# Performance work log

Hardware: AMD Instinct MI355X
Metric: run time of the kernel (lower is better)

The kernel has to match this reference:

```python
import jax, jax.numpy as jnp
import numpy as np

ROI = 268
K = 32
SLOPE = 0.33
EPS = 1e-5

def leaky(h):
    return jnp.where(h >= 0, h, SLOPE * h)

def bn(h, g, b):
    # BatchNorm in training mode: biased batch statistics over the node/batch axis
    mu = h.mean(0)
    var = ((h - mu) ** 2).mean(0)
    return (h - mu) * jax.lax.rsqrt(var + EPS) * g + b


def setup_inputs():
    B, F, C, deg = 64, ROI, 32, 32
    N = B * ROI
    key = jax.random.key(0)
    ks = jax.random.split(key, 32)
    x = jax.random.normal(ks[0], (N, F), jnp.float32)
    # static within-graph edges: every node has exactly `deg` incoming edges
    tgt = jnp.repeat(jnp.arange(N, dtype=jnp.int32), deg)
    src = (tgt // ROI) * ROI + jax.random.randint(ks[1], (N * deg,), 0, ROI, dtype=jnp.int32)
    edge_index = jnp.stack([src, tgt])
    batch = jnp.repeat(jnp.arange(B, dtype=jnp.int32), ROI)
    def lin(k, i, o):
        return 0.05 * jax.random.normal(k, (i, o), jnp.float32)
    def vec(k, o):
        return 0.05 * jax.random.normal(k, (o,), jnp.float32)
    p = dict(
        x=x, edge_index=edge_index, batch=batch,
        W1a=lin(ks[2], 2 * F, C), b1a=vec(ks[3], C), W1b=lin(ks[4], C, C), b1b=vec(ks[5], C),
        g1=1.0 + vec(ks[6], C), be1=vec(ks[7], C),
        W2a=lin(ks[8], 2 * F, C), b2a=vec(ks[9], C), W2b=lin(ks[10], C, C), b2b=vec(ks[11], C),
        g2=1.0 + vec(ks[12], C), be2=vec(ks[13], C),
        W3=lin(ks[14], 2 * F, 1), b3=vec(ks[15], 1), g3=1.0 + vec(ks[16], 1), be3=vec(ks[17], 1),
        Wl1=lin(ks[18], ROI + 2 * C, 256), bl1=vec(ks[19], 256), g4=1.0 + vec(ks[20], 256), be4=vec(ks[21], 256),
        Wl2=lin(ks[22], 256, 128), bl2=vec(ks[23], 128), g5=1.0 + vec(ks[24], 128), be5=vec(ks[25], 128),
        Wl3=lin(ks[26], 128, 1), bl3=vec(ks[27], 1),
    )
    return p


def reference(x, edge_index, batch,
              W1a, b1a, W1b, b1b, g1, be1,
              W2a, b2a, W2b, b2b, g2, be2,
              W3, b3, g3, be3,
              Wl1, bl1, g4, be4, Wl2, bl2, g5, be5, Wl3, bl3):
    N, F = x.shape
    B = N // ROI
    src, tgt = edge_index[0], edge_index[1]
    xi = x[tgt]                       # [E, F] central node feature
    xd = x[src] - xi                  # [E, F] x_j - x_i
    # --- gcn1: EdgeConv(mlp1) + BN + LeakyReLU (dropout = identity in eval) ---
    m1 = leaky(xi @ W1a[:F] + xd @ W1a[F:] + b1a) @ W1b + b1b   # [E, C]
    a1 = jax.ops.segment_max(m1, tgt, num_segments=N)
    a1 = jnp.where(jnp.isfinite(a1), a1, 0.0)
    x1 = leaky(bn(a1, g1, be1))
    # --- gcn3: EdgeConv(mlp3) + BN + LeakyReLU ---
    m3 = xi @ W3[:F] + xd @ W3[F:] + b3                          # [E, 1]
    a3 = jax.ops.segment_max(m3, tgt, num_segments=N)
    a3 = jnp.where(jnp.isfinite(a3), a3, 0.0)
    x3 = leaky(bn(a3, g3, be3))
    # --- gcn2: DynamicEdgeConv(mlp2, k=32) + BN + LeakyReLU ---
    xg = x.reshape(B, ROI, F)
    sq = jnp.sum(xg * xg, -1)
    d2 = sq[:, :, None] + sq[:, None, :] - 2.0 * jnp.einsum('bif,bjf->bij', xg, xg)
    _, idx = jax.lax.top_k(-d2, K)                               # [B, ROI, K], includes self
    xj = jax.vmap(lambda f, i: f[i])(xg, idx)                    # [B, ROI, K, F]
    part_i = jnp.einsum('bif,fc->bic', xg, W2a[:F])
    part_d = jnp.einsum('bikf,fc->bikc', xj - xg[:, :, None, :], W2a[F:])
    h2 = leaky(part_i[:, :, None, :] + part_d + b2a)
    m2 = h2 @ W2b + b2b                                          # [B, ROI, K, C]
    x2 = leaky(bn(m2.max(axis=2).reshape(N, -1), g2, be2))
    # --- readout ---
    counts = jax.ops.segment_sum(jnp.ones((N, 1), x.dtype), batch, num_segments=B)
    p1 = jax.ops.segment_sum(x1, batch, num_segments=B) / counts
    p2 = jax.ops.segment_sum(x2, batch, num_segments=B) / counts
    z = jnp.concatenate([p1, p2, x3.reshape(B, ROI)], -1)        # [B, 268+64]
    z = leaky(bn(z @ Wl1 + bl1, g4, be4))
    z = leaky(bn(z @ Wl2 + bl2, g5, be5))
    return z @ Wl3 + bl3                                          # [B, 1]
```

## Files before the change

### kernel.cpp

```cpp
#include <hip/hip_runtime.h>
#include <hip/hip_bf16.h>

#define ROI   268
#define FDIM  268
#define NB    64
#define NN    (NB*ROI)
#define CC    32
#define DEG   32
#define KSEL  32
#define SLOPE 0.33f
#define EPSBN 1e-5f

typedef __attribute__((ext_vector_type(8)))  short bf16x8;
typedef __attribute__((ext_vector_type(4)))  float f32x4;
typedef __attribute__((ext_vector_type(16))) float f32x16;

__device__ __forceinline__ float lrelu(float h) { return h >= 0.f ? h : SLOPE * h; }

__device__ __forceinline__ unsigned short f2bf(float f) {
    union { __hip_bfloat16 h; unsigned short s; } u;
    u.h = __float2bfloat16(f);
    return u.s;
}
__device__ __forceinline__ float bf2f(unsigned short h) {
    return __uint_as_float(((unsigned int)h) << 16);
}

#define PREP_PACK_BLOCKS  2448
#define PREP_PACKW_BLOCKS 18
#define PREP_SCAL_BLOCKS  1072

__global__ __launch_bounds__(256) void k_prep(
    const float* __restrict__ x,
    const float* __restrict__ W1a, const float* __restrict__ W2a,
    const float* __restrict__ W3,  const float* __restrict__ b3,
    unsigned short* __restrict__ Xh, unsigned short* __restrict__ Xl,
    unsigned short* __restrict__ Wfh, unsigned short* __restrict__ Wfl,
    float* __restrict__ u3, float* __restrict__ v3, float* __restrict__ sqv)
{
    const int bid = blockIdx.x;
    const int tid = threadIdx.x;
    if (bid < PREP_PACK_BLOCKS) {
        const int gid = bid * 256 + tid;
        const int l   = gid & 63;
        const int f3  = gid >> 6;
        const int ks  = f3 % 9;
        const int bc  = f3 / 9;
        const int ct  = bc % 17;
        const int b   = bc / 17;
        const int node = ct * 16 + (l & 15);
        const int k0   = ks * 32 + (l >> 4) * 8;
        float f[8];
        #pragma unroll
        for (int j = 0; j < 8; ++j) f[j] = 0.f;
        if (node < ROI) {
            const float* row = &x[((size_t)b * ROI + node) * FDIM];
            if (k0 + 3 < FDIM) { float4 v = *(const float4*)&row[k0];     f[0]=v.x; f[1]=v.y; f[2]=v.z; f[3]=v.w; }
            if (k0 + 7 < FDIM) { float4 v = *(const float4*)&row[k0 + 4]; f[4]=v.x; f[5]=v.y; f[6]=v.z; f[7]=v.w; }
        }
        unsigned short hh[8], ll[8];
        #pragma unroll
        for (int j = 0; j < 8; ++j) {
            hh[j] = f2bf(f[j]);
            ll[j] = f2bf(f[j] - bf2f(hh[j]));
        }
        uint4 hp, lp;
        hp.x = (unsigned)hh[0] | ((unsigned)hh[1] << 16); hp.y = (unsigned)hh[2] | ((unsigned)hh[3] << 16);
        hp.z = (unsigned)hh[4] | ((unsigned)hh[5] << 16); hp.w = (unsigned)hh[6] | ((unsigned)hh[7] << 16);
        lp.x = (unsigned)ll[0] | ((unsigned)ll[1] << 16); lp.y = (unsigned)ll[2] | ((unsigned)ll[3] << 16);
        lp.z = (unsigned)ll[4] | ((unsigned)ll[5] << 16); lp.w = (unsigned)ll[6] | ((unsigned)ll[7] << 16);
        const size_t base = (size_t)f3 * 512 + l * 8;
        *(uint4*)&Xh[base] = hp;
        *(uint4*)&Xl[base] = lp;
    } else if (bid < PREP_PACK_BLOCKS + PREP_PACKW_BLOCKS) {
        const int gid = (bid - PREP_PACK_BLOCKS) * 256 + tid;
        const int l  = gid & 63;
        const int f3 = gid >> 6;
        const int ks = f3 % 9;
        const int mc = f3 / 9;
        const int ct = mc & 1;
        const int m  = mc >> 1;
        const int k0 = ks * 32 + (l >> 4) * 8;
        const int c  = ct * 16 + (l & 15);
        const float* W = (m < 2) ? W1a : W2a;
        const bool isU = (m & 1) == 0;
        unsigned short hh[8], ll[8];
        #pragma unroll
        for (int j = 0; j < 8; ++j) {
            const int kk = k0 + j;
            float val = 0.f;
            if (kk < FDIM) {
                float wb = W[(size_t)(FDIM + kk) * CC + c];
                val = isU ? (W[(size_t)kk * CC + c] - wb) : wb;
            }
            hh[j] = f2bf(val);
            ll[j] = f2bf(val - bf2f(hh[j]));
        }
        uint4 hp, lp;
        hp.x = (unsigned)hh[0] | ((unsigned)hh[1] << 16); hp.y = (unsigned)hh[2] | ((unsigned)hh[3] << 16);
        hp.z = (unsigned)hh[4] | ((unsigned)hh[5] << 16); hp.w = (unsigned)hh[6] | ((unsigned)hh[7] << 16);
        lp.x = (unsigned)ll[0] | ((unsigned)ll[1] << 16); lp.y = (unsigned)ll[2] | ((unsigned)ll[3] << 16);
        lp.z = (unsigned)ll[4] | ((unsigned)ll[5] << 16); lp.w = (unsigned)ll[6] | ((unsigned)ll[7] << 16);
        const size_t base = (size_t)f3 * 512 + l * 8;
        *(uint4*)&Wfh[base] = hp;
        *(uint4*)&Wfl[base] = lp;
    } else {
        const int s = bid - (PREP_PACK_BLOCKS + PREP_PACKW_BLOCKS);
        const int l = tid & 63;
        #pragma unroll
        for (int i = 0; i < 4; ++i) {
            const int n = s * 16 + i * 4 + (tid >> 6);
            const float* row = &x[(size_t)n * FDIM];
            float su = 0.f, sv = 0.f, sq = 0.f;
            #pragma unroll
            for (int t = 0; t < 4; ++t) {
                const int f = l + 64 * t;
                float xv = row[f];
                float wv = W3[FDIM + f];
                float wu = W3[f] - wv;
                su += xv * wu; sv += xv * wv; sq += xv * xv;
            }
            if (l < 12) {
                const int f = 256 + l;
                float xv = row[f];
                float wv = W3[FDIM + f];
                float wu = W3[f] - wv;
                su += xv * wu; sv += xv * wv; sq += xv * xv;
            }
            #pragma unroll
            for (int mm = 32; mm > 0; mm >>= 1) {
                su += __shfl_xor(su, mm);
                sv += __shfl_xor(sv, mm);
                sq += __shfl_xor(sq, mm);
            }
            if (l == 0) {
                u3[n] = su + b3[0];
                v3[n] = sv;
                sqv[n] = sq;
            }
        }
    }
}

__global__ __launch_bounds__(256) void k_proj_mfma(
    const unsigned short* __restrict__ Xh, const unsigned short* __restrict__ Xl,
    const unsigned short* __restrict__ Wfh, const unsigned short* __restrict__ Wfl,
    const float* __restrict__ b1a, const float* __restrict__ b2a,
    float* __restrict__ u1, float* __restrict__ v1,
    float* __restrict__ u2, float* __restrict__ v2)
{
    const int tid = threadIdx.x;
    const int l   = tid & 63;
    const int m   = tid >> 6;
    const int tile = blockIdx.x;
    const int b    = tile / 17;
    const int ctn  = tile % 17;

    bf16x8 Ah[9], Al[9];
    {
        const size_t abase = (size_t)tile * 9 * 512 + l * 8;
        #pragma unroll
        for (int ks = 0; ks < 9; ++ks) {
            Ah[ks] = *(const bf16x8*)&Xh[abase + ks * 512];
            Al[ks] = *(const bf16x8*)&Xl[abase + ks * 512];
        }
    }
    float* outp = (m == 0) ? u1 : (m == 1) ? v1 : (m == 2) ? u2 : v2;

    #pragma unroll
    for (int ct = 0; ct < 2; ++ct) {
        const size_t wbase = ((size_t)((m * 2 + ct) * 9)) * 512 + l * 8;
        f32x4 acc = {0.f, 0.f, 0.f, 0.f};
        #pragma unroll
        for (int ks = 0; ks < 9; ++ks) {
            bf16x8 bh = *(const bf16x8*)&Wfh[wbase + ks * 512];
            bf16x8 bl = *(const bf16x8*)&Wfl[wbase + ks * 512];
            acc = __builtin_amdgcn_mfma_f32_16x16x32_bf16(Ah[ks], bh, acc, 0, 0, 0);
            acc = __builtin_amdgcn_mfma_f32_16x16x32_bf16(Ah[ks], bl, acc, 0, 0, 0);
            acc = __builtin_amdgcn_mfma_f32_16x16x32_bf16(Al[ks], bh, acc, 0, 0, 0);
        }
        const int ch = ct * 16 + (l & 15);
        float bias = 0.f;
        if (m == 0) bias = b1a[ch];
        else if (m == 2) bias = b2a[ch];
        const int r0 = (l >> 4) * 4;
        #pragma unroll
        for (int i = 0; i < 4; ++i) {
            const int node = ctn * 16 + r0 + i;
            if (node < ROI)
                outp[((size_t)b * ROI + node) * 32 + ch] = acc[i] + bias;
        }
    }
}

__global__ __launch_bounds__(256) void k_dist(
    const unsigned short* __restrict__ Xh, const unsigned short* __restrict__ Xl,
    const float* __restrict__ sqv, float* __restrict__ d2)
{
    __shared__ float sqj[288];
    __shared__ float sqr[32];
    const int tid = threadIdx.x;
    const int b   = blockIdx.y;
    const int r0g = blockIdx.x * 32;
    const size_t bN = (size_t)b * ROI;

    for (int t = tid; t < 288; t += 256)
        sqj[t] = (t < ROI) ? sqv[bN + t] : __builtin_inff();
    if (tid < 32) sqr[tid] = (r0g + tid < ROI) ? sqv[bN + r0g + tid] : 0.f;

    const int l  = tid & 63;
    const int w  = tid >> 6;
    const int ra = w & 1;
    const int rtile = min(blockIdx.x * 2 + ra, 16);

    bf16x8 Ah[9], Al[9];
    {
        const size_t abase = ((size_t)(b * 17 + rtile) * 9) * 512 + l * 8;
        #pragma unroll
        for (int ks = 0; ks < 9; ++ks) {
            Ah[ks] = *(const bf16x8*)&Xh[abase + ks * 512];
            Al[ks] = *(const bf16x8*)&Xl[abase + ks * 512];
        }
    }
    __syncthreads();

    float* drow = &d2[(size_t)b * 288 * 288];
    for (int ct = (w >> 1); ct < 17; ct += 2) {
        const size_t bbase = ((size_t)(b * 17 + ct) * 9) * 512 + l * 8;
        f32x4 acc = {0.f, 0.f, 0.f, 0.f};
        #pragma unroll
        for (int ks = 0; ks < 9; ++ks) {
            bf16x8 bh = *(const bf16x8*)&Xh[bbase + ks * 512];
            bf16x8 bl = *(const bf16x8*)&Xl[bbase + ks * 512];
            acc = __builtin_amdgcn_mfma_f32_16x16x32_bf16(Ah[ks], bh, acc, 0, 0, 0);
            acc = __builtin_amdgcn_mfma_f32_16x16x32_bf16(Ah[ks], bl, acc, 0, 0, 0);
            acc = __builtin_amdgcn_mfma_f32_16x16x32_bf16(Al[ks], bh, acc, 0, 0, 0);
        }
        const int col = ct * 16 + (l & 15);
        const float sj = sqj[col];
        const int rr = ra * 16 + (l >> 4) * 4;
        #pragma unroll
        for (int i = 0; i < 4; ++i)
            drow[(size_t)(r0g + rr + i) * 288 + col] = sqr[rr + i] + sj - 2.f * acc[i];
    }
    for (int t = tid; t < 32 * 16; t += 256) {
        const int r = t >> 4, cc = 272 + (t & 15);
        drow[(size_t)(r0g + r) * 288 + cc] = __builtin_inff();
    }
}

__global__ __launch_bounds__(256) void k_sel(
    const float* __restrict__ d2, int* __restrict__ knn)
{
    const int grp = blockIdx.x * 8 + (threadIdx.x >> 5);
    const int sl  = threadIdx.x & 31;
    const int b   = grp / ROI;
    const int row = grp - b * ROI;
    const float* src = &d2[((size_t)b * 288 + row) * 288];

    unsigned k[9];
    #pragma unroll
    for (int q = 0; q < 9; ++q) {
        const int idx = q * 32 + sl;
        unsigned bits = __float_as_uint(src[idx]);
        unsigned msk  = (unsigned)(((int)bits) >> 31) | 0x80000000u;
        k[q] = ((bits ^ msk) & ~0x1FFu) | (unsigned)idx;
    }
    #pragma unroll
    for (int i = 1; i < 9; ++i) {
        #pragma unroll
        for (int j = i; j > 0; --j) {
            unsigned lo = k[j-1] < k[j] ? k[j-1] : k[j];
            unsigned hi = k[j-1] < k[j] ? k[j]   : k[j-1];
            k[j-1] = lo; k[j] = hi;
        }
    }
    unsigned keep = 0;
    #pragma unroll
    for (int it = 0; it < KSEL; ++it) {
        unsigned m = k[0];
        #pragma unroll
        for (int mm = 16; mm > 0; mm >>= 1) {
            unsigned o = (unsigned)__shfl_xor((int)m, mm, 32);
            m = o < m ? o : m;
        }
        if (sl == it) keep = m;
        const bool win = (k[0] == m);
        #pragma unroll
        for (int q = 0; q < 8; ++q) k[q] = win ? k[q+1] : k[q];
        k[8] = win ? 0xFFFFFFFFu : k[8];
    }
    knn[(size_t)grp * KSEL + sl] = b * ROI + (int)(keep & 0x1FFu);
}

__global__ __launch_bounds__(256) void k_edge_both(
    const float* __restrict__ u1, const float* __restrict__ v1,
    const float* __restrict__ W1b, const float* __restrict__ b1b,
    const int* __restrict__ ei,
    const float* __restrict__ u2, const float* __restrict__ v2,
    const float* __restrict__ W2b, const float* __restrict__ b2b,
    const int* __restrict__ knn,
    const float* __restrict__ u3, const float* __restrict__ v3,
    float* __restrict__ a1, float* __restrict__ a2, float* __restrict__ a3)
{
    const int tid  = threadIdx.x;
    const int l    = tid & 63;
    const int wv   = tid >> 6;
    const int half = l >> 5;
    const int e    = l & 31;
    const bool g1 = blockIdx.x < (NN / 16);
    const int  nb = g1 ? blockIdx.x : blockIdx.x - (NN / 16);
    const float* u  = g1 ? u1 : u2;
    const float* v  = g1 ? v1 : v2;
    const float* Wb = g1 ? W1b : W2b;
    const float* bb = g1 ? b1b : b2b;
    const int* nbr  = g1 ? ei : knn;
    float* aout     = g1 ? a1 : a2;

    union { bf16x8 v8; unsigned u4[4]; } B0, B1;
    #pragma unroll
    for (int j = 0; j < 4; ++j) {
        B0.u4[j] = (unsigned)f2bf(Wb[(half * 8 + 2*j    ) * 32 + e])
                 | ((unsigned)f2bf(Wb[(half * 8 + 2*j + 1) * 32 + e]) << 16);
        B1.u4[j] = (unsigned)f2bf(Wb[(16 + half * 8 + 2*j    ) * 32 + e])
                 | ((unsigned)f2bf(Wb[(16 + half * 8 + 2*j + 1) * 32 + e]) << 16);
    }
    const float biasc = bb[e];

    for (int nn = 0; nn < 4; ++nn) {
        const int n  = nb * 16 + wv * 4 + nn;
        const int jn = nbr[(size_t)n * DEG + e];

        float hv[16];
        #pragma unroll
        for (int s = 0; s < 2; ++s) {
            const int c0 = s * 16 + half * 8;
            float4 uv0 = *(const float4*)&u[(size_t)n  * 32 + c0];
            float4 uv1 = *(const float4*)&u[(size_t)n  * 32 + c0 + 4];
            float4 vv0 = *(const float4*)&v[(size_t)jn * 32 + c0];
            float4 vv1 = *(const float4*)&v[(size_t)jn * 32 + c0 + 4];
            hv[s*8+0] = lrelu(uv0.x + vv0.x);
            hv[s*8+1] = lrelu(uv0.y + vv0.y);
            hv[s*8+2] = lrelu(uv0.z + vv0.z);
            hv[s*8+3] = lrelu(uv0.w + vv0.w);
            hv[s*8+4] = lrelu(uv1.x + vv1.x);
            hv[s*8+5] = lrelu(uv1.y + vv1.y);
            hv[s*8+6] = lrelu(uv1.z + vv1.z);
            hv[s*8+7] = lrelu(uv1.w + vv1.w);
        }
        union { bf16x8 v8; unsigned u4[4]; } A0, A1;
        #pragma unroll
        for (int j = 0; j < 4; ++j) {
            A0.u4[j] = (unsigned)f2bf(hv[2*j])     | ((unsigned)f2bf(hv[2*j + 1]) << 16);
            A1.u4[j] = (unsigned)f2bf(hv[8 + 2*j]) | ((unsigned)f2bf(hv[8 + 2*j + 1]) << 16);
        }
        f32x16 acc = {0.f,0.f,0.f,0.f,0.f,0.f,0.f,0.f,0.f,0.f,0.f,0.f,0.f,0.f,0.f,0.f};
        acc = __builtin_amdgcn_mfma_f32_32x32x16_bf16(A0.v8, B0.v8, acc, 0, 0, 0);
        acc = __builtin_amdgcn_mfma_f32_32x32x16_bf16(A1.v8, B1.v8, acc, 0, 0, 0);

        float mx = acc[0];
        #pragma unroll
        for (int r = 1; r < 16; ++r) mx = fmaxf(mx, acc[r]);
        mx = fmaxf(mx, __shfl_xor(mx, 32));
        if (l < 32) aout[(size_t)n * 32 + l] = mx + biasc;

        if (g1) {
            float a3v = u3[n] + v3[jn];
            #pragma unroll
            for (int mm = 16; mm > 0; mm >>= 1) a3v = fmaxf(a3v, __shfl_xor(a3v, mm));
            if (l == 0) a3[n] = a3v;
        }
    }
}

__global__ __launch_bounds__(256) void k_stats1(
    const float* __restrict__ a1, const float* __restrict__ a2,
    float* __restrict__ part)
{
    const int p = blockIdx.x;
    const int tid = threadIdx.x;
    const int ch = tid & 31, sub = tid >> 5;
    const size_t base = (size_t)p * ROI;
    float s1 = 0.f, q1 = 0.f, s2 = 0.f, q2 = 0.f;
    for (int n = sub; n < ROI; n += 8) {
        float v1 = a1[(base + n) * 32 + ch];
        float v2 = a2[(base + n) * 32 + ch];
        s1 += v1; q1 += v1 * v1; s2 += v2; q2 += v2 * v2;
    }
    __shared__ float L[4][256];
    L[0][tid] = s1; L[1][tid] = q1; L[2][tid] = s2; L[3][tid] = q2;
    __syncthreads();
    if (tid < 128) {
        const int a = tid >> 5, c = tid & 31;
        float s = 0.f;
        #pragma unroll
        for (int k = 0; k < 8; ++k) s += L[a][c + 32 * k];
        part[p * 128 + a * 32 + c] = s;
    }
}

__global__ __launch_bounds__(256) void k_stats2(
    const float* __restrict__ part, const float* __restrict__ a3,
    const float* __restrict__ g1, const float* __restrict__ be1,
    const float* __restrict__ g2, const float* __restrict__ be2,
    const float* __restrict__ g3, const float* __restrict__ be3,
    float* __restrict__ st)
{
    const int tid = threadIdx.x;
    float p0 = 0.f, p1 = 0.f, p2 = 0.f, p3 = 0.f;
    float q0 = 0.f, q1 = 0.f, q2 = 0.f, q3 = 0.f;
    int n = tid;
    for (; n + 768 < NN; n += 1024) {
        float a = a3[n], b = a3[n + 256], c = a3[n + 512], d = a3[n + 768];
        p0 += a; q0 += a * a;
        p1 += b; q1 += b * b;
        p2 += c; q2 += c * c;
        p3 += d; q3 += d * d;
    }
    for (; n < NN; n += 256) { float a = a3[n]; p0 += a; q0 += a * a; }
    float s = (p0 + p1) + (p2 + p3);
    float q = (q0 + q1) + (q2 + q3);
    __shared__ float S3[256], Q3[256];
    S3[tid] = s; Q3[tid] = q; __syncthreads();
    for (int off = 128; off > 0; off >>= 1) {
        if (tid < off) { S3[tid] += S3[tid + off]; Q3[tid] += Q3[tid + off]; }
        __syncthreads();
    }
    if (tid < 64) {
        const int a = (tid >> 5) * 2, c = tid & 31;
        float s0 = 0.f, s1 = 0.f, q0b = 0.f, q1b = 0.f;
        for (int p = 0; p < 64; p += 2) {
            s0  += part[p * 128 + a * 32 + c];
            q0b += part[p * 128 + (a + 1) * 32 + c];
            s1  += part[(p + 1) * 128 + a * 32 + c];
            q1b += part[(p + 1) * 128 + (a + 1) * 32 + c];
        }
        float ss = s0 + s1, qq = q0b + q1b;
        float gv = (tid < 32) ? g1[c] : g2[c];
        float bv = (tid < 32) ? be1[c] : be2[c];
        float mu  = ss * (1.f / NN);
        float var = qq * (1.f / NN) - mu * mu;
        float sc  = gv * rsqrtf(var + EPSBN);
        st[tid * 2] = sc; st[tid * 2 + 1] = bv - mu * sc;
    }
    if (tid == 64) {
        float mu  = S3[0] * (1.f / NN);
        float var = Q3[0] * (1.f / NN) - mu * mu;
        float sc  = g3[0] * rsqrtf(var + EPSBN);
        st[128] = sc; st[129] = be3[0] - mu * sc;
    }
}

__global__ __launch_bounds__(256) void k_pool_fc1(
    const float* __restrict__ a1, const float* __restrict__ a2, const float* __restrict__ a3,
    const float* __restrict__ st, const float* __restrict__ Wl1, const float* __restrict__ bl1,
    float* __restrict__ h1)
{
    const int b = blockIdx.x, tid = threadIdx.x;
    __shared__ float zs[332];
    __shared__ float P[4][64];
    const int c = tid & 63, grp = tid >> 6;
    const float* src = (c < 32) ? a1 : a2;
    const int ch = c & 31;
    const float sc = st[c * 2], sh = st[c * 2 + 1];
    {
        const size_t rb = (size_t)b * ROI;
        float p0 = 0.f, p1 = 0.f, p2 = 0.f, p3 = 0.f;
        int i = grp;
        for (; i + 12 < ROI; i += 16) {
            p0 += lrelu(src[(rb + i)      * 32 + ch] * sc + sh);
            p1 += lrelu(src[(rb + i + 4)  * 32 + ch] * sc + sh);
            p2 += lrelu(src[(rb + i + 8)  * 32 + ch] * sc + sh);
            p3 += lrelu(src[(rb + i + 12) * 32 + ch] * sc + sh);
        }
        for (; i < ROI; i += 4)
            p0 += lrelu(src[(rb + i) * 32 + ch] * sc + sh);
        P[grp][c] = (p0 + p1) + (p2 + p3);
    }
    const float sc3 = st[128], sh3 = st[129];
    for (int i = tid; i < ROI; i += 256)
        zs[64 + i] = lrelu(a3[b * ROI + i] * sc3 + sh3);
    __syncthreads();
    if (tid < 64)
        zs[tid] = (P[0][tid] + P[1][tid] + P[2][tid] + P[3][tid]) * (1.f / ROI);
    __syncthreads();
    {
        float s0 = 0.f, s1 = 0.f, s2 = 0.f, s3 = 0.f;
        #pragma unroll 4
        for (int k = 0; k < 332; k += 4) {
            s0 += zs[k]     * Wl1[(size_t)k       * 256 + tid];
            s1 += zs[k + 1] * Wl1[(size_t)(k + 1) * 256 + tid];
            s2 += zs[k + 2] * Wl1[(size_t)(k + 2) * 256 + tid];
            s3 += zs[k + 3] * Wl1[(size_t)(k + 3) * 256 + tid];
        }
        h1[(size_t)b * 256 + tid] = bl1[tid] + ((s0 + s1) + (s2 + s3));
    }
}

__global__ __launch_bounds__(128) void k_fc2s(
    const float* __restrict__ h1,
    const float* __restrict__ g4, const float* __restrict__ be4,
    const float* __restrict__ Wl2, const float* __restrict__ bl2,
    float* __restrict__ h2)
{
    const int b = blockIdx.x, tid = threadIdx.x;
    __shared__ float hs[256];
    float s0 = 0.f, q0 = 0.f, s1 = 0.f, q1 = 0.f;
    float s2 = 0.f, q2 = 0.f, s3 = 0.f, q3 = 0.f;
    for (int r = 0; r < NB; r += 2) {
        float a = h1[(size_t)r * 256 + tid];
        float c = h1[(size_t)r * 256 + tid + 128];
        float d = h1[(size_t)(r + 1) * 256 + tid];
        float e = h1[(size_t)(r + 1) * 256 + tid + 128];
        s0 += a; q0 += a * a;
        s1 += c; q1 += c * c;
        s2 += d; q2 += d * d;
        s3 += e; q3 += e * e;
    }
    {
        float ssA = s0 + s2, qqA = q0 + q2;
        float muA = ssA * (1.f / NB);
        float vaA = qqA * (1.f / NB) - muA * muA;
        float scA = g4[tid] * rsqrtf(vaA + EPSBN);
        float shA = be4[tid] - muA * scA;
        hs[tid] = lrelu(h1[(size_t)b * 256 + tid] * scA + shA);
        float ssB = s1 + s3, qqB = q1 + q3;
        float muB = ssB * (1.f / NB);
        float vaB = qqB * (1.f / NB) - muB * muB;
        float scB = g4[tid + 128] * rsqrtf(vaB + EPSBN);
        float shB = be4[tid + 128] - muB * scB;
        hs[tid + 128] = lrelu(h1[(size_t)b * 256 + tid + 128] * scB + shB);
    }
    __syncthreads();
    float s0b = 0.f, s1b = 0.f, s2b = 0.f, s3b = 0.f;
    #pragma unroll 4
    for (int k = 0; k < 256; k += 4) {
        s0b += hs[k]     * Wl2[(size_t)k       * 128 + tid];
        s1b += hs[k + 1] * Wl2[(size_t)(k + 1) * 128 + tid];
        s2b += hs[k + 2] * Wl2[(size_t)(k + 2) * 128 + tid];
        s3b += hs[k + 3] * Wl2[(size_t)(k + 3) * 128 + tid];
    }
    h2[(size_t)b * 128 + tid] = bl2[tid] + ((s0b + s1b) + (s2b + s3b));
}

__global__ __launch_bounds__(128) void k_fc3s(
    const float* __restrict__ h2,
    const float* __restrict__ g5, const float* __restrict__ be5,
    const float* __restrict__ Wl3, const float* __restrict__ bl3,
    float* __restrict__ out)
{
    const int tid = threadIdx.x;
    __shared__ float T[64][133];
    float s0 = 0.f, q0 = 0.f, s1 = 0.f, q1 = 0.f;
    for (int r = 0; r < NB; r += 2) {
        float a = h2[(size_t)r * 128 + tid];
        float b = h2[(size_t)(r + 1) * 128 + tid];
        s0 += a; q0 += a * a;
        s1 += b; q1 += b * b;
    }
    float ss = s0 + s1, qq = q0 + q1;
    float mu  = ss * (1.f / NB);
    float var = qq * (1.f / NB) - mu * mu;
    float sc  = g5[tid] * rsqrtf(var + EPSBN);
    float sh  = be5[tid] - mu * sc;
    const float w3 = Wl3[tid];
    for (int r = 0; r < NB; ++r)
        T[r][tid] = lrelu(h2[(size_t)r * 128 + tid] * sc + sh) * w3;
    __syncthreads();
    if (tid < 64) {
        float a0 = 0.f, a1 = 0.f, a2 = 0.f, a3 = 0.f;
        #pragma unroll 4
        for (int c = 0; c < 128; c += 4) {
            a0 += T[tid][c];
            a1 += T[tid][c + 1];
            a2 += T[tid][c + 2];
            a3 += T[tid][c + 3];
        }
        out[tid] = bl3[0] + ((a0 + a1) + (a2 + a3));
    }
}

extern "C" void kernel_launch(void* const* d_in, const int* in_sizes, int n_in,
                              void* d_out, int out_size, void* d_ws, size_t ws_size,
                              hipStream_t stream)
{
    (void)in_sizes; (void)n_in; (void)out_size; (void)ws_size;
    const float* x   = (const float*)d_in[0];
    const int*   ei  = (const int*)d_in[1];
    const float* W1a = (const float*)d_in[3];
    const float* b1a = (const float*)d_in[4];
    const float* W1b = (const float*)d_in[5];
    const float* b1b = (const float*)d_in[6];
    const float* g1  = (const float*)d_in[7];
    const float* be1 = (const float*)d_in[8];
    const float* W2a = (const float*)d_in[9];
    const float* b2a = (const float*)d_in[10];
    const float* W2b = (const float*)d_in[11];
    const float* b2b = (const float*)d_in[12];
    const float* g2  = (const float*)d_in[13];
    const float* be2 = (const float*)d_in[14];
    const float* W3  = (const float*)d_in[15];
    const float* b3  = (const float*)d_in[16];
    const float* g3  = (const float*)d_in[17];
    const float* be3 = (const float*)d_in[18];
    const float* Wl1 = (const float*)d_in[19];
    const float* bl1 = (const float*)d_in[20];
    const float* g4  = (const float*)d_in[21];
    const float* be4 = (const float*)d_in[22];
    const float* Wl2 = (const float*)d_in[23];
    const float* bl2 = (const float*)d_in[24];
    const float* g5  = (const float*)d_in[25];
    const float* be5 = (const float*)d_in[26];
    const float* Wl3 = (const float*)d_in[27];
    const float* bl3 = (const float*)d_in[28];

    float* ws  = (float*)d_ws;
    float* u1  = ws;
    float* v1  = u1 + (size_t)NN * 32;
    float* u2  = v1 + (size_t)NN * 32;
    float* v2  = u2 + (size_t)NN * 32;
    float* u3  = v2 + (size_t)NN * 32;
    float* v3  = u3 + NN;
    float* sqv = v3 + NN;
    float* a1  = sqv + NN;
    float* a2  = a1 + (size_t)NN * 32;
    float* a3  = a2 + (size_t)NN * 32;
    int*   knn = (int*)(a3 + NN);
    float* st  = (float*)(knn + (size_t)NN * 32);
    float* z   = st + 130;
    float* h1  = z + (size_t)NB * 332;
    float* h2  = h1 + (size_t)NB * 256;
    float* s4  = h2 + (size_t)NB * 128;
    float* s5  = s4 + 512;
    float* part = s5 + 512;
    unsigned short* Xh = (unsigned short*)(((uintptr_t)(part + 64 * 128) + 255) & ~(uintptr_t)255);
    unsigned short* Xl = Xh + (size_t)64 * 17 * 9 * 512;
    float* d2 = (float*)(((uintptr_t)(Xl + (size_t)64 * 17 * 9 * 512) + 255) & ~(uintptr_t)255);
    unsigned short* Wfh = (unsigned short*)(d2 + (size_t)64 * 288 * 288);
    unsigned short* Wfl = Wfh + (size_t)8 * 9 * 512;

    k_prep<<<PREP_PACK_BLOCKS + PREP_PACKW_BLOCKS + PREP_SCAL_BLOCKS, 256, 0, stream>>>(
        x, W1a, W2a, W3, b3, Xh, Xl, Wfh, Wfl, u3, v3, sqv);
    k_proj_mfma<<<1088, 256, 0, stream>>>(Xh, Xl, Wfh, Wfl, b1a, b2a, u1, v1, u2, v2);
    k_dist<<<dim3(9, NB), 256, 0, stream>>>(Xh, Xl, sqv, d2);
    k_sel<<<NN / 8, 256, 0, stream>>>(d2, knn);
    k_edge_both<<<2 * (NN / 16), 256, 0, stream>>>(u1, v1, W1b, b1b, ei,
                                                   u2, v2, W2b, b2b, knn,
                                                   u3, v3, a1, a2, a3);
    k_stats1<<<64, 256, 0, stream>>>(a1, a2, part);
    k_stats2<<<1, 256, 0, stream>>>(part, a3, g1, be1, g2, be2, g3, be3, st);
    k_pool_fc1<<<NB, 256, 0, stream>>>(a1, a2, a3, st, Wl1, bl1, h1);
    k_fc2s<<<NB, 128, 0, stream>>>(h1, g4, be4, Wl2, bl2, h2);
    k_fc3s<<<1, 128, 0, stream>>>(h2, g5, be5, Wl3, bl3, (float*)d_out);
}
```

Measured before the change: 161.1 us.

## Fuse projection and distance kernels, merge BN stats into pool, prefetch neighbor indices

Merges the projection GEMM and pairwise-distance GEMM into one launch, with block ranges split by blockIdx. The distance part now stages each column tile in LDS and has four waves share it across four row tiles. Folds the single-block BN-statistics kernel into the per-graph pool/FC1 kernel, so every block recomputes the a3 reduction redundantly. Also hoists neighbor-index loads ahead of the edge loop. Together these cut launches and global B-tile traffic, at the cost of extra syncs and duplicated reduction work.

```diff
diff --git a/kernel.cpp b/kernel.cpp
--- a/kernel.cpp
+++ b/kernel.cpp
@@ -142,110 +142,121 @@
     }
 }
 
-__global__ __launch_bounds__(256) void k_proj_mfma(
+#define PD_DIST_BLOCKS 320
+#define PD_PROJ_BLOCKS 1088
+
+__global__ __launch_bounds__(256) void k_projdist(
     const unsigned short* __restrict__ Xh, const unsigned short* __restrict__ Xl,
     const unsigned short* __restrict__ Wfh, const unsigned short* __restrict__ Wfl,
     const float* __restrict__ b1a, const float* __restrict__ b2a,
+    const float* __restrict__ sqv,
     float* __restrict__ u1, float* __restrict__ v1,
-    float* __restrict__ u2, float* __restrict__ v2)
-{
+    float* __restrict__ u2, float* __restrict__ v2,
+    float* __restrict__ d2)
+{
+    __shared__ __align__(16) unsigned short Bh_l[4608], Bl_l[4608];
+    __shared__ float sqj[288];
     const int tid = threadIdx.x;
     const int l   = tid & 63;
-    const int m   = tid >> 6;
-    const int tile = blockIdx.x;
-    const int b    = tile / 17;
-    const int ctn  = tile % 17;
+    const int w   = tid >> 6;
+
+    if (blockIdx.x >= PD_DIST_BLOCKS) {
+        const int tile = blockIdx.x - PD_DIST_BLOCKS;
+        const int b    = tile / 17;
+        const int ctn  = tile % 17;
+        bf16x8 Ah[9], Al[9];
+        {
+            const size_t abase = (size_t)tile * 9 * 512 + l * 8;
+            #pragma unroll
+            for (int ks = 0; ks < 9; ++ks) {
+                Ah[ks] = *(const bf16x8*)&Xh[abase + ks * 512];
+                Al[ks] = *(const bf16x8*)&Xl[abase + ks * 512];
+            }
+        }
+        float* outp = (w == 0) ? u1 : (w == 1) ? v1 : (w == 2) ? u2 : v2;
+        #pragma unroll
+        for (int ct = 0; ct < 2; ++ct) {
+            const size_t wbase = ((size_t)((w * 2 + ct) * 9)) * 512 + l * 8;
+            f32x4 acc = {0.f, 0.f, 0.f, 0.f};
+            #pragma unroll
+            for (int ks = 0; ks < 9; ++ks) {
+                bf16x8 bh = *(const bf16x8*)&Wfh[wbase + ks * 512];
+                bf16x8 bl = *(const bf16x8*)&Wfl[wbase + ks * 512];
+                acc = __builtin_amdgcn_mfma_f32_16x16x32_bf16(Ah[ks], bh, acc, 0, 0, 0);
+                acc = __builtin_amdgcn_mfma_f32_16x16x32_bf16(Ah[ks], bl, acc, 0, 0, 0);
+                acc = __builtin_amdgcn_mfma_f32_16x16x32_bf16(Al[ks], bh, acc, 0, 0, 0);
+            }
+            const int ch = ct * 16 + (l & 15);
+            float bias = 0.f;
+            if (w == 0) bias = b1a[ch];
+            else if (w == 2) bias = b2a[ch];
+            const int r0 = (l >> 4) * 4;
+            #pragma unroll
+            for (int i = 0; i < 4; ++i) {
+                const int node = ctn * 16 + r0 + i;
+                if (node < ROI)
+                    outp[((size_t)b * ROI + node) * 32 + ch] = acc[i] + bias;
+            }
+        }
+        return;
+    }
+
+    const int bid = blockIdx.x;
+    const int b   = bid / 5;
+    const int bx  = bid % 5;
+    const int at  = min(bx * 4 + w, 16);
+    const size_t bN = (size_t)b * ROI;
+
+    for (int t = tid; t < 288; t += 256)
+        sqj[t] = (t < ROI) ? sqv[bN + t] : __builtin_inff();
 
     bf16x8 Ah[9], Al[9];
     {
-        const size_t abase = (size_t)tile * 9 * 512 + l * 8;
+        const size_t abase = ((size_t)(b * 17 + at) * 9) * 512 + l * 8;
         #pragma unroll
         for (int ks = 0; ks < 9; ++ks) {
             Ah[ks] = *(const bf16x8*)&Xh[abase + ks * 512];
             Al[ks] = *(const bf16x8*)&Xl[abase + ks * 512];
         }
     }
-    float* outp = (m == 0) ? u1 : (m == 1) ? v1 : (m == 2) ? u2 : v2;
-
+    const int rbase = at * 16 + (l >> 4) * 4;
+    float sqr4[4];
     #pragma unroll
-    for (int ct = 0; ct < 2; ++ct) {
-        const size_t wbase = ((size_t)((m * 2 + ct) * 9)) * 512 + l * 8;
+    for (int i = 0; i < 4; ++i) {
+        const int row = rbase + i;
+        sqr4[i] = (row < ROI) ? sqv[bN + row] : 0.f;
+    }
+
+    float* drow = &d2[(size_t)b * 288 * 288];
+    for (int ct = 0; ct < 17; ++ct) {
+        __syncthreads();
+        {
+            const unsigned short* srcH = &Xh[((size_t)(b * 17 + ct) * 9) * 512];
+            const unsigned short* srcL = &Xl[((size_t)(b * 17 + ct) * 9) * 512];
+            for (int t = tid; t < 576; t += 256) {
+                *(uint4*)&Bh_l[t * 8] = *(const uint4*)&srcH[t * 8];
+                *(uint4*)&Bl_l[t * 8] = *(const uint4*)&srcL[t * 8];
+            }
+        }
+        __syncthreads();
         f32x4 acc = {0.f, 0.f, 0.f, 0.f};
         #pragma unroll
         for (int ks = 0; ks < 9; ++ks) {
-            bf16x8 bh = *(const bf16x8*)&Wfh[wbase + ks * 512];
-            bf16x8 bl = *(const bf16x8*)&Wfl[wbase + ks * 512];
+            bf16x8 bh = *(const bf16x8*)&Bh_l[ks * 512 + l * 8];
+            bf16x8 bl = *(const bf16x8*)&Bl_l[ks * 512 + l * 8];
             acc = __builtin_amdgcn_mfma_f32_16x16x32_bf16(Ah[ks], bh, acc, 0, 0, 0);
             acc = __builtin_amdgcn_mfma_f32_16x16x32_bf16(Ah[ks], bl, acc, 0, 0, 0);
             acc = __builtin_amdgcn_mfma_f32_16x16x32_bf16(Al[ks], bh, acc, 0, 0, 0);
         }
-        const int ch = ct * 16 + (l & 15);
-        float bias = 0.f;
-        if (m == 0) bias = b1a[ch];
-        else if (m == 2) bias = b2a[ch];
-        const int r0 = (l >> 4) * 4;
-        #pragma unroll
-        for (int i = 0; i < 4; ++i) {
-            const int node = ctn * 16 + r0 + i;
-            if (node < ROI)
-                outp[((size_t)b * ROI + node) * 32 + ch] = acc[i] + bias;
-        }
-    }
-}
-
-__global__ __launch_bounds__(256) void k_dist(
-    const unsigned short* __restrict__ Xh, const unsigned short* __restrict__ Xl,
-    const float* __restrict__ sqv, float* __restrict__ d2)
-{
-    __shared__ float sqj[288];
-    __shared__ float sqr[32];
-    const int tid = threadIdx.x;
-    const int b   = blockIdx.y;
-    const int r0g = blockIdx.x * 32;
-    const size_t bN = (size_t)b * ROI;
-
-    for (int t = tid; t < 288; t += 256)
-        sqj[t] = (t < ROI) ? sqv[bN + t] : __builtin_inff();
-    if (tid < 32) sqr[tid] = (r0g + tid < ROI) ? sqv[bN + r0g + tid] : 0.f;
-
-    const int l  = tid & 63;
-    const int w  = tid >> 6;
-    const int ra = w & 1;
-    const int rtile = min(blockIdx.x * 2 + ra, 16);
-
-    bf16x8 Ah[9], Al[9];
-    {
-        const size_t abase = ((size_t)(b * 17 + rtile) * 9) * 512 + l * 8;
-        #pragma unroll
-        for (int ks = 0; ks < 9; ++ks) {
-            Ah[ks] = *(const bf16x8*)&Xh[abase + ks * 512];
-            Al[ks] = *(const bf16x8*)&Xl[abase + ks * 512];
-        }
-    }
-    __syncthreads();
-
-    float* drow = &d2[(size_t)b * 288 * 288];
-    for (int ct = (w >> 1); ct < 17; ct += 2) {
-        const size_t bbase = ((size_t)(b * 17 + ct) * 9) * 512 + l * 8;
-        f32x4 acc = {0.f, 0.f, 0.f, 0.f};
-        #pragma unroll
-        for (int ks = 0; ks < 9; ++ks) {
-            bf16x8 bh = *(const bf16x8*)&Xh[bbase + ks * 512];
-            bf16x8 bl = *(const bf16x8*)&Xl[bbase + ks * 512];
-            acc = __builtin_amdgcn_mfma_f32_16x16x32_bf16(Ah[ks], bh, acc, 0, 0, 0);
-            acc = __builtin_amdgcn_mfma_f32_16x16x32_bf16(Ah[ks], bl, acc, 0, 0, 0);
-            acc = __builtin_amdgcn_mfma_f32_16x16x32_bf16(Al[ks], bh, acc, 0, 0, 0);
-        }
         const int col = ct * 16 + (l & 15);
         const float sj = sqj[col];
-        const int rr = ra * 16 + (l >> 4) * 4;
         #pragma unroll
         for (int i = 0; i < 4; ++i)
-            drow[(size_t)(r0g + rr + i) * 288 + col] = sqr[rr + i] + sj - 2.f * acc[i];
-    }
-    for (int t = tid; t < 32 * 16; t += 256) {
-        const int r = t >> 4, cc = 272 + (t & 15);
-        drow[(size_t)(r0g + r) * 288 + cc] = __builtin_inff();
+            drow[(size_t)(rbase + i) * 288 + col] = sqr4[i] + sj - 2.f * acc[i];
+    }
+    for (int t = tid; t < 64 * 16; t += 256) {
+        const int r = bx * 64 + (t >> 4);
+        if (r < 288) drow[(size_t)r * 288 + 272 + (t & 15)] = __builtin_inff();
     }
 }
 
@@ -327,9 +338,15 @@
     }
     const float biasc = bb[e];
 
+    int jns[4];
+    #pragma unroll
+    for (int nn = 0; nn < 4; ++nn)
+        jns[nn] = nbr[(size_t)(nb * 16 + wv * 4 + nn) * DEG + e];
+
+    #pragma unroll 2
     for (int nn = 0; nn < 4; ++nn) {
         const int n  = nb * 16 + wv * 4 + nn;
-        const int jn = nbr[(size_t)n * DEG + e];
+        const int jn = jns[nn];
 
         float hv[16];
         #pragma unroll
@@ -399,29 +416,37 @@
     }
 }
 
-__global__ __launch_bounds__(256) void k_stats2(
-    const float* __restrict__ part, const float* __restrict__ a3,
+__global__ __launch_bounds__(256) void k_pool_fc1(
+    const float* __restrict__ a1, const float* __restrict__ a2, const float* __restrict__ a3,
+    const float* __restrict__ part,
     const float* __restrict__ g1, const float* __restrict__ be1,
     const float* __restrict__ g2, const float* __restrict__ be2,
     const float* __restrict__ g3, const float* __restrict__ be3,
-    float* __restrict__ st)
-{
-    const int tid = threadIdx.x;
-    float p0 = 0.f, p1 = 0.f, p2 = 0.f, p3 = 0.f;
-    float q0 = 0.f, q1 = 0.f, q2 = 0.f, q3 = 0.f;
-    int n = tid;
-    for (; n + 768 < NN; n += 1024) {
-        float a = a3[n], b = a3[n + 256], c = a3[n + 512], d = a3[n + 768];
-        p0 += a; q0 += a * a;
-        p1 += b; q1 += b * b;
-        p2 += c; q2 += c * c;
-        p3 += d; q3 += d * d;
-    }
-    for (; n < NN; n += 256) { float a = a3[n]; p0 += a; q0 += a * a; }
-    float s = (p0 + p1) + (p2 + p3);
-    float q = (q0 + q1) + (q2 + q3);
+    const float* __restrict__ Wl1, const float* __restrict__ bl1,
+    float* __restrict__ h1)
+{
+    const int b = blockIdx.x, tid = threadIdx.x;
+    __shared__ float stl[130];
+    __shared__ float zs[332];
+    __shared__ float P[4][64];
     __shared__ float S3[256], Q3[256];
-    S3[tid] = s; Q3[tid] = q; __syncthreads();
+
+    {
+        float p0 = 0.f, p1 = 0.f, p2 = 0.f, p3 = 0.f;
+        float q0 = 0.f, q1 = 0.f, q2 = 0.f, q3 = 0.f;
+        int n = tid;
+        for (; n + 768 < NN; n += 1024) {
+            float a = a3[n], bb = a3[n + 256], c = a3[n + 512], d = a3[n + 768];
+            p0 += a; q0 += a * a;
+            p1 += bb; q1 += bb * bb;
+            p2 += c; q2 += c * c;
+            p3 += d; q3 += d * d;
+        }
+        for (; n < NN; n += 256) { float a = a3[n]; p0 += a; q0 += a * a; }
+        S3[tid] = (p0 + p1) + (p2 + p3);
+        Q3[tid] = (q0 + q1) + (q2 + q3);
+    }
+    __syncthreads();
     for (int off = 128; off > 0; off >>= 1) {
         if (tid < off) { S3[tid] += S3[tid + off]; Q3[tid] += Q3[tid + off]; }
         __syncthreads();
@@ -441,28 +466,20 @@
         float mu  = ss * (1.f / NN);
         float var = qq * (1.f / NN) - mu * mu;
         float sc  = gv * rsqrtf(var + EPSBN);
-        st[tid * 2] = sc; st[tid * 2 + 1] = bv - mu * sc;
+        stl[tid * 2] = sc; stl[tid * 2 + 1] = bv - mu * sc;
     }
     if (tid == 64) {
         float mu  = S3[0] * (1.f / NN);
         float var = Q3[0] * (1.f / NN) - mu * mu;
         float sc  = g3[0] * rsqrtf(var + EPSBN);
-        st[128] = sc; st[129] = be3[0] - mu * sc;
-    }
-}
-
-__global__ __launch_bounds__(256) void k_pool_fc1(
-    const float* __restrict__ a1, const float* __restrict__ a2, const float* __restrict__ a3,
-    const float* __restrict__ st, const float* __restrict__ Wl1, const float* __restrict__ bl1,
-    float* __restrict__ h1)
-{
-    const int b = blockIdx.x, tid = threadIdx.x;
-    __shared__ float zs[332];
-    __shared__ float P[4][64];
+        stl[128] = sc; stl[129] = be3[0] - mu * sc;
+    }
+    __syncthreads();
+
     const int c = tid & 63, grp = tid >> 6;
     const float* src = (c < 32) ? a1 : a2;
     const int ch = c & 31;
-    const float sc = st[c * 2], sh = st[c * 2 + 1];
+    const float sc = stl[c * 2], sh = stl[c * 2 + 1];
     {
         const size_t rb = (size_t)b * ROI;
         float p0 = 0.f, p1 = 0.f, p2 = 0.f, p3 = 0.f;
@@ -477,13 +494,14 @@
             p0 += lrelu(src[(rb + i) * 32 + ch] * sc + sh);
         P[grp][c] = (p0 + p1) + (p2 + p3);
     }
-    const float sc3 = st[128], sh3 = st[129];
+    const float sc3 = stl[128], sh3 = stl[129];
     for (int i = tid; i < ROI; i += 256)
         zs[64 + i] = lrelu(a3[b * ROI + i] * sc3 + sh3);
     __syncthreads();
     if (tid < 64)
         zs[tid] = (P[0][tid] + P[1][tid] + P[2][tid] + P[3][tid]) * (1.f / ROI);
     __syncthreads();
+
     {
         float s0 = 0.f, s1 = 0.f, s2 = 0.f, s3 = 0.f;
         #pragma unroll 4
@@ -626,13 +644,9 @@
     float* a2  = a1 + (size_t)NN * 32;
     float* a3  = a2 + (size_t)NN * 32;
     int*   knn = (int*)(a3 + NN);
-    float* st  = (float*)(knn + (size_t)NN * 32);
-    float* z   = st + 130;
-    float* h1  = z + (size_t)NB * 332;
+    float* h1  = (float*)(knn + (size_t)NN * 32);
     float* h2  = h1 + (size_t)NB * 256;
-    float* s4  = h2 + (size_t)NB * 128;
-    float* s5  = s4 + 512;
-    float* part = s5 + 512;
+    float* part = h2 + (size_t)NB * 128;
     unsigned short* Xh = (unsigned short*)(((uintptr_t)(part + 64 * 128) + 255) & ~(uintptr_t)255);
     unsigned short* Xl = Xh + (size_t)64 * 17 * 9 * 512;
     float* d2 = (float*)(((uintptr_t)(Xl + (size_t)64 * 17 * 9 * 512) + 255) & ~(uintptr_t)255);
@@ -641,15 +655,15 @@
 
     k_prep<<<PREP_PACK_BLOCKS + PREP_PACKW_BLOCKS + PREP_SCAL_BLOCKS, 256, 0, stream>>>(
         x, W1a, W2a, W3, b3, Xh, Xl, Wfh, Wfl, u3, v3, sqv);
-    k_proj_mfma<<<1088, 256, 0, stream>>>(Xh, Xl, Wfh, Wfl, b1a, b2a, u1, v1, u2, v2);
-    k_dist<<<dim3(9, NB), 256, 0, stream>>>(Xh, Xl, sqv, d2);
+    k_projdist<<<PD_DIST_BLOCKS + PD_PROJ_BLOCKS, 256, 0, stream>>>(
+        Xh, Xl, Wfh, Wfl, b1a, b2a, sqv, u1, v1, u2, v2, d2);
     k_sel<<<NN / 8, 256, 0, stream>>>(d2, knn);
     k_edge_both<<<2 * (NN / 16), 256, 0, stream>>>(u1, v1, W1b, b1b, ei,
                                                    u2, v2, W2b, b2b, knn,
                                                    u3, v3, a1, a2, a3);
     k_stats1<<<64, 256, 0, stream>>>(a1, a2, part);
-    k_stats2<<<1, 256, 0, stream>>>(part, a3, g1, be1, g2, be2, g3, be3, st);
-    k_pool_fc1<<<NB, 256, 0, stream>>>(a1, a2, a3, st, Wl1, bl1, h1);
+    k_pool_fc1<<<NB, 256, 0, stream>>>(a1, a2, a3, part, g1, be1, g2, be2, g3, be3,
+                                       Wl1, bl1, h1);
     k_fc2s<<<NB, 128, 0, stream>>>(h1, g4, be4, Wl2, bl2, h2);
     k_fc3s<<<1, 128, 0, stream>>>(h2, g5, be5, Wl3, bl3, (float*)d_out);
 }
```

Result: faster. 147.5 us (-8.4%).
